# Kernel optimization log

Hardware: AMD Instinct MI355X
Metric: run time of the kernel (lower is better)

## Reference

```python
import jax, jax.numpy as jnp
import numpy as np

NEG_INF = -1e20

# Dims: s=512 samples, b=2048 background, t=32 trees, f=64 features, h=128 hidden, y=1
S, B, T, F, H, Y = 512, 2048, 32, 64, 128, 1


def setup_inputs() -> dict:
    key = jax.random.key(0)
    ks = jax.random.split(key, 8)
    X = jax.random.normal(ks[0], (S, F), dtype=jnp.float32)
    background_X = jax.random.normal(ks[1], (B, F), dtype=jnp.float32)
    background_y = jax.random.normal(ks[2], (B, Y), dtype=jnp.float32)
    neighbors_hot = jax.random.randint(ks[3], (S, B, T), 0, 2).astype(jnp.bool_)
    # encoder params: Linear(F->H), Tanh, Linear(H->H)  (n_layers=2)
    W1 = jax.random.normal(ks[4], (F, H), dtype=jnp.float32) / np.sqrt(F)
    b1 = jnp.zeros((H,), dtype=jnp.float32)
    W2 = jax.random.normal(ks[5], (H, H), dtype=jnp.float32) / np.sqrt(H)
    b2 = jnp.zeros((H,), dtype=jnp.float32)
    return {"X": X, "background_X": background_X, "background_y": background_y,
            "neighbors_hot": neighbors_hot, "W1": W1, "b1": b1, "W2": W2, "b2": b2}


def reference(X, background_X, background_y, neighbors_hot, W1, b1, W2, b2):
    def encode(x):
        return jnp.tanh(x @ W1 + b1) @ W2 + b2  # Linear-Tanh-Linear

    X_enc = encode(X)                    # (s, h)
    bg_enc = encode(background_X)        # (b, h)
    dots = X_enc @ bg_enc.T              # (s, b)
    # broadcast over trees + mask, softmax over background axis
    scores = jnp.where(neighbors_hot, dots[:, :, None], NEG_INF)  # (s, b, t)
    first_alphas = jax.nn.softmax(scores, axis=1)                 # (s, b, t)
    first_leaf_xs = jnp.einsum('sbt,bf->stf', first_alphas, background_X)
    first_leaf_y = jnp.einsum('sbt,by->sty', first_alphas, background_y)
    return first_leaf_xs, first_leaf_y, first_alphas
```

## Files before the change

### kernel.cpp

```cpp
#include <hip/hip_runtime.h>
#include <hip/hip_bf16.h>

#define NS 512
#define NB 2048
#define NT 32
#define NF 64
#define NH 128
#define NFX 80
#define PSTR 81

#define OY  ((size_t)NS * NT * NF)
#define OA  (OY + (size_t)NS * NT)

#define ENC_B  1280
#define TR_B   32

typedef __attribute__((ext_vector_type(8))) short bf16x8;
typedef __attribute__((ext_vector_type(4))) float f32x4;

__device__ __forceinline__ unsigned short f2bfu(float x) {
    __hip_bfloat16 h = __float2bfloat16(x);
    return __builtin_bit_cast(unsigned short, h);
}

__device__ __forceinline__ unsigned int pack16_bytes(uint4 v) {
    unsigned int r = 0;
    unsigned int xs[4] = {v.x, v.y, v.z, v.w};
    #pragma unroll
    for (int i = 0; i < 4; ++i) {
        unsigned int x = xs[i];
        unsigned int t = (x | ((x & 0x7F7F7F7Fu) + 0x7F7F7F7Fu)) & 0x80808080u;
        t >>= 7;
        unsigned int n = (t | (t >> 7) | (t >> 14) | (t >> 21)) & 0xFu;
        r |= n << (i * 4);
    }
    return r;
}

__global__ __launch_bounds__(256) void prep2_k(
        const float* __restrict__ X, const float* __restrict__ bgX,
        const float* __restrict__ bgy,
        const float* __restrict__ W1, const float* __restrict__ b1,
        const float* __restrict__ W2, const float* __restrict__ b2,
        float* __restrict__ enc, unsigned short* __restrict__ bgXT2) {
    __shared__ float cbuf[64 * 65];
    const int blk = blockIdx.x;
    const int tid = threadIdx.x;

    if (blk < ENC_B) {
        const int r0 = blk * 2;
        float* xr = cbuf;
        float* hr = cbuf + 128;
        if (tid < 128) {
            int r = tid >> 6, c = tid & 63;
            int row = r0 + r;
            const float* src = (row < NS) ? (X + (size_t)row * NF)
                                          : (bgX + (size_t)(row - NS) * NF);
            xr[r * 64 + c] = src[c];
        }
        __syncthreads();
        const int j = tid & 127, h = tid >> 7;
        const float* xh = xr + h * 64;
        float a1 = b1[j];
        #pragma unroll 4
        for (int f = 0; f < NF; ++f)
            a1 = fmaf(xh[f], W1[f * NH + j], a1);
        hr[h * 128 + j] = tanhf(a1);
        __syncthreads();
        const float* hh = hr + h * 128;
        float a2 = b2[j];
        #pragma unroll 4
        for (int k = 0; k < NH; ++k)
            a2 = fmaf(hh[k], W2[k * NH + j], a2);
        enc[(size_t)(r0 + h) * NH + j] = a2;
        return;
    }

    {
        const int bb0 = blk - ENC_B;
        const int b0 = bb0 * 64;
        float (*t_lds)[65] = (float(*)[65])cbuf;
        #pragma unroll
        for (int it = 0; it < 4; ++it) {
            int idx = (it * 256 + tid) * 4;
            int r = idx >> 6, c = idx & 63;
            *(float4*)(&t_lds[r][c]) = *(const float4*)(bgX + (size_t)(b0 + r) * NF + c);
        }
        __syncthreads();
        uint4* fb = (uint4*)bgXT2;
        const int c2 = tid >> 7;
        const int cg = bb0 * 2 + c2;
        for (int idx = tid & 127; idx < 320; idx += 128) {
            const int n = idx >> 6, l = idx & 63;
            const int lo = l & 15, hi = l >> 4;
            union { unsigned short u[8]; uint4 q; } pk;
            if (n < 4) {
                #pragma unroll
                for (int jj = 0; jj < 8; ++jj)
                    pk.u[jj] = f2bfu(t_lds[c2 * 32 + hi * 8 + jj][n * 16 + lo]);
            } else {
                #pragma unroll
                for (int jj = 0; jj < 8; ++jj) {
                    if (lo == 0)      pk.u[jj] = f2bfu(bgy[b0 + c2 * 32 + hi * 8 + jj]);
                    else if (lo == 1) pk.u[jj] = 0x3F80;
                    else              pk.u[jj] = 0;
                }
            }
            fb[((size_t)cg * 5 + n) * 64 + l] = pk.q;
        }
    }
}

__global__ __launch_bounds__(256) void dots_k(const float* __restrict__ Xe,
        const float* __restrict__ Be, float* __restrict__ dots) {
    __shared__ float At[64 * 68];
    __shared__ float Bt[64 * 68];
    const int s0 = blockIdx.y * 64, b0 = blockIdx.x * 64;
    const int tid = threadIdx.x;
    const int ts = tid >> 4, tb = tid & 15;
    float acc[4][4] = {};
    for (int kt = 0; kt < 2; ++kt) {
        __syncthreads();
        #pragma unroll
        for (int it = 0; it < 4; ++it) {
            int idx = tid * 4 + it * 1024;
            int r = idx >> 6, k = idx & 63;
            *(float4*)(&At[r * 68 + k]) = *(const float4*)(Xe + (size_t)(s0 + r) * NH + kt * 64 + k);
            float4 bvv = *(const float4*)(Be + (size_t)(b0 + r) * NH + kt * 64 + k);
            Bt[(k + 0) * 68 + r] = bvv.x;
            Bt[(k + 1) * 68 + r] = bvv.y;
            Bt[(k + 2) * 68 + r] = bvv.z;
            Bt[(k + 3) * 68 + r] = bvv.w;
        }
        __syncthreads();
        #pragma unroll 4
        for (int k = 0; k < 64; ++k) {
            float4 bq = *(const float4*)(&Bt[k * 68 + tb * 4]);
            float a[4];
            #pragma unroll
            for (int i = 0; i < 4; ++i) a[i] = At[(ts + 16 * i) * 68 + k];
            #pragma unroll
            for (int i = 0; i < 4; ++i) {
                acc[i][0] = fmaf(a[i], bq.x, acc[i][0]);
                acc[i][1] = fmaf(a[i], bq.y, acc[i][1]);
                acc[i][2] = fmaf(a[i], bq.z, acc[i][2]);
                acc[i][3] = fmaf(a[i], bq.w, acc[i][3]);
            }
        }
    }
    #pragma unroll
    for (int i = 0; i < 4; ++i) {
        float4 v = make_float4(acc[i][0], acc[i][1], acc[i][2], acc[i][3]);
        *(float4*)(&dots[(size_t)(s0 + ts + 16 * i) * NB + b0 + tb * 4]) = v;
    }
}

__global__ __launch_bounds__(256) void fusedA_k(const void* __restrict__ mask,
        float* __restrict__ dots, const unsigned short* __restrict__ bgXT2,
        unsigned int* __restrict__ pmask32,
        float* __restrict__ rden_g, float* __restrict__ out) {
    __shared__ __align__(16) unsigned int mrow[NB];
    __shared__ __align__(16) unsigned short e_bf[NB];
    __shared__ float part[3 * NT * PSTR];
    __shared__ float wmax[4];
    __shared__ float rden_l[NT];
    __shared__ float ytmp[NT];

    const int s = blockIdx.x;
    const int tid = threadIdx.x;
    const int lane = tid & 63, w = tid >> 6;
    const int lo = lane & 15, hi = lane >> 4;

    float* drow = dots + (size_t)s * NB;
    float4 d0 = *(const float4*)(drow + tid * 8);
    float4 d1 = *(const float4*)(drow + tid * 8 + 4);
    int isbyte;
    {
        uint4 v = ((const uint4*)mask)[w * 64 + lane];
        isbyte = (__ballot(((v.x | v.y | v.z | v.w) & 0xFFFFFF00u) != 0u) != 0ull);
    }
    if (isbyte) {
        const char* base = (const char*)mask + (size_t)s * 65536 + w * 16384;
        #pragma unroll 4
        for (int k = 0; k < 16; ++k) {
            uint4 q = *(const uint4*)(base + k * 1024 + lane * 16);
            unsigned int p = pack16_bytes(q);
            unsigned int p1 = (unsigned int)__shfl_down((int)p, 1, 64);
            if ((lane & 1) == 0)
                mrow[w * 512 + k * 32 + (lane >> 1)] = p | (p1 << 16);
        }
    } else {
        const char* base = (const char*)mask + (size_t)s * 262144 + w * 65536;
        for (int k = 0; k < 64; ++k) {
            uint4 v = *(const uint4*)(base + k * 1024 + lane * 16);
            unsigned int r = (v.x ? 1u : 0u) | (v.y ? 2u : 0u) |
                             (v.z ? 4u : 0u) | (v.w ? 8u : 0u);
            r |= ((unsigned int)__shfl_down((int)r, 1, 64)) << 4;
            r |= ((unsigned int)__shfl_down((int)r, 2, 64)) << 8;
            r |= ((unsigned int)__shfl_down((int)r, 4, 64)) << 16;
            if ((lane & 7) == 0)
                mrow[w * 512 + k * 8 + (lane >> 3)] = r;
        }
    }

    float pmax = fmaxf(fmaxf(fmaxf(d0.x, d0.y), fmaxf(d0.z, d0.w)),
                       fmaxf(fmaxf(d1.x, d1.y), fmaxf(d1.z, d1.w)));
    #pragma unroll
    for (int off = 32; off >= 1; off >>= 1)
        pmax = fmaxf(pmax, __shfl_xor(pmax, off, 64));
    if (lane == 0) wmax[w] = pmax;
    __syncthreads();
    const float Ms = fmaxf(fmaxf(wmax[0], wmax[1]), fmaxf(wmax[2], wmax[3]));
    float ev[8] = {d0.x, d0.y, d0.z, d0.w, d1.x, d1.y, d1.z, d1.w};
    union { unsigned short u[8]; uint4 q; } epk;
    #pragma unroll
    for (int q = 0; q < 8; ++q) { ev[q] = __expf(ev[q] - Ms); epk.u[q] = f2bfu(ev[q]); }
    *(float4*)(drow + tid * 8)     = make_float4(ev[0], ev[1], ev[2], ev[3]);
    *(float4*)(drow + tid * 8 + 4) = make_float4(ev[4], ev[5], ev[6], ev[7]);
    *(uint4*)(&e_bf[tid * 8]) = epk.q;
    unsigned int* pmg = pmask32 + (size_t)s * NB;
    *(uint4*)(pmg + tid * 4)          = *(const uint4*)(&mrow[tid * 4]);
    *(uint4*)(pmg + (tid + 256) * 4)  = *(const uint4*)(&mrow[(tid + 256) * 4]);
    __syncthreads();

    f32x4 acc[2][5] = {};
    const uint4* fb = (const uint4*)bgXT2;
    #pragma unroll 2
    for (int ks = 0; ks < 16; ++ks) {
        const int bb = w * 512 + ks * 32 + hi * 8;
        uint4 ew4 = *(const uint4*)(&e_bf[bb]);
        uint4 m0 = *(const uint4*)(&mrow[bb]);
        uint4 m1 = *(const uint4*)(&mrow[bb + 4]);
        unsigned int ew[4] = {ew4.x, ew4.y, ew4.z, ew4.w};
        unsigned int mv[8] = {m0.x, m0.y, m0.z, m0.w, m1.x, m1.y, m1.z, m1.w};
        unsigned int A0[4], A1[4];
        #pragma unroll
        for (int p = 0; p < 4; ++p) {
            unsigned int mlo = mv[2 * p]     >> lo;
            unsigned int mhi = mv[2 * p + 1] >> lo;
            unsigned int k0 = ((mlo & 1u)       ? 0x0000FFFFu : 0u) |
                              ((mhi & 1u)       ? 0xFFFF0000u : 0u);
            unsigned int k1 = ((mlo & 0x10000u) ? 0x0000FFFFu : 0u) |
                              ((mhi & 0x10000u) ? 0xFFFF0000u : 0u);
            A0[p] = ew[p] & k0;
            A1[p] = ew[p] & k1;
        }
        bf16x8 a0 = __builtin_bit_cast(bf16x8, make_uint4(A0[0], A0[1], A0[2], A0[3]));
        bf16x8 a1 = __builtin_bit_cast(bf16x8, make_uint4(A1[0], A1[1], A1[2], A1[3]));
        const uint4* fr = fb + ((size_t)(w * 16 + ks) * 5) * 64 + lane;
        #pragma unroll
        for (int n = 0; n < 5; ++n) {
            uint4 bv = fr[n * 64];
            bf16x8 bfr = __builtin_bit_cast(bf16x8, bv);
            acc[0][n] = __builtin_amdgcn_mfma_f32_16x16x32_bf16(a0, bfr, acc[0][n], 0, 0, 0);
            acc[1][n] = __builtin_amdgcn_mfma_f32_16x16x32_bf16(a1, bfr, acc[1][n], 0, 0, 0);
        }
    }

    if (w > 0) {
        #pragma unroll
        for (int m = 0; m < 2; ++m)
            #pragma unroll
            for (int n = 0; n < 5; ++n)
                #pragma unroll
                for (int r = 0; r < 4; ++r) {
                    int t = m * 16 + hi * 4 + r, f = n * 16 + lo;
                    part[(w - 1) * (NT * PSTR) + t * PSTR + f] = acc[m][n][r];
                }
    }
    __syncthreads();
    if (w == 0) {
        #pragma unroll
        for (int m = 0; m < 2; ++m)
            #pragma unroll
            for (int r = 0; r < 4; ++r) {
                int t = m * 16 + hi * 4 + r;
                int o = t * PSTR + 64 + lo;
                float tot = acc[m][4][r] + part[o] + part[NT * PSTR + o] + part[2 * NT * PSTR + o];
                if (lo == 0) ytmp[t] = tot;
                if (lo == 1) rden_l[t] = (tot > 0.f) ? 1.f / tot : 0.f;
            }
    }
    __syncthreads();
    if (w == 0) {
        float* xout = out + (size_t)s * NT * NF;
        #pragma unroll
        for (int m = 0; m < 2; ++m)
            #pragma unroll
            for (int n = 0; n < 4; ++n)
                #pragma unroll
                for (int r = 0; r < 4; ++r) {
                    int t = m * 16 + hi * 4 + r, f = n * 16 + lo;
                    int o = t * PSTR + f;
                    float tot = acc[m][n][r] + part[o] + part[NT * PSTR + o] + part[2 * NT * PSTR + o];
                    xout[t * NF + f] = tot * rden_l[t];
                }
    }
    if (tid < 32) {
        out[OY + (size_t)s * NT + tid] = ytmp[tid] * rden_l[tid];
        rden_g[(size_t)s * NT + tid] = rden_l[tid];
    }
}

__global__ __launch_bounds__(256) void alphas_k(const float* __restrict__ e,
        const unsigned int* __restrict__ pmask32, const float* __restrict__ rden_g,
        float* __restrict__ out) {
    const int tid = threadIdx.x;
    const int blk = blockIdx.x;
    const int s = blk >> 3;
    const int tq = tid & 7;
    const f32x4 rd4 = *(const f32x4*)(rden_g + (size_t)s * NT + tq * 4);
    const float* erow = e + (size_t)s * NB;
    const unsigned int* mr = pmask32 + (size_t)s * NB;
    float* aout = out + OA + (size_t)s * NB * NT;
    const int b0 = (blk & 7) * 256 + (tid >> 3);

    float ev[8];
    unsigned int mv[8];
    #pragma unroll
    for (int j = 0; j < 8; ++j) {
        ev[j] = erow[b0 + j * 32];
        mv[j] = mr[b0 + j * 32] >> (tq * 4);
    }
    #pragma unroll
    for (int j = 0; j < 8; ++j) {
        const int b = b0 + j * 32;
        f32x4 v;
        v.x = (mv[j] & 1u) ? ev[j] * rd4.x : 0.f;
        v.y = (mv[j] & 2u) ? ev[j] * rd4.y : 0.f;
        v.z = (mv[j] & 4u) ? ev[j] * rd4.z : 0.f;
        v.w = (mv[j] & 8u) ? ev[j] * rd4.w : 0.f;
        *(f32x4*)(aout + (size_t)b * NT + tq * 4) = v;
    }
}

extern "C" void kernel_launch(void* const* d_in, const int* in_sizes, int n_in,
                              void* d_out, int out_size, void* d_ws, size_t ws_size,
                              hipStream_t stream) {
    (void)in_sizes; (void)n_in; (void)out_size; (void)ws_size;
    const float* X   = (const float*)d_in[0];
    const float* bgX = (const float*)d_in[1];
    const float* bgy = (const float*)d_in[2];
    const void*  nh  = d_in[3];
    const float* W1  = (const float*)d_in[4];
    const float* b1v = (const float*)d_in[5];
    const float* W2  = (const float*)d_in[6];
    const float* b2v = (const float*)d_in[7];
    float* out = (float*)d_out;
    char* ws = (char*)d_ws;

    float* enc = (float*)(ws + 4096);
    float* rden_g = (float*)(ws + 4096);
    float* Xe = enc;
    float* Be = enc + (size_t)NS * NH;
    float* dots = (float*)(ws + 4096 + (size_t)(NS + NB) * NH * 4);
    unsigned int* pmask32 = (unsigned int*)((char*)dots + (size_t)NS * NB * 4);
    unsigned short* bgXT2 = (unsigned short*)((char*)pmask32 + (size_t)NS * NB * 4);

    prep2_k<<<ENC_B + TR_B, 256, 0, stream>>>(X, bgX, bgy, W1, b1v, W2, b2v, enc, bgXT2);
    dots_k<<<dim3(NB / 64, NS / 64), 256, 0, stream>>>(Xe, Be, dots);
    fusedA_k<<<NS, 256, 0, stream>>>(nh, dots, bgXT2, pmask32, rden_g, out);
    alphas_k<<<NS * 8, 256, 0, stream>>>(dots, pmask32, rden_g, out);
}
```

Baseline: 115.2 us.

## Drop packed-mask buffer; reread raw mask in alphas kernel and shrink reduction LDS

fusedA_k no longer writes a packed per-sample bitmask to global memory. alphas_k now rereads the original byte or int mask directly, which removes the pmask32 round trip and a barrier. The cross-wave partial reduction uses one LDS buffer reused over three sequential rounds instead of three buffers, cutting LDS use to raise occupancy at the cost of extra barriers. The mask loads in fusedA_k are batched eight at a time to get more loads in flight. In exchange alphas_k reads the full byte mask (32 MB) rather than the 4 MB packed copy.

New measurement: 123.9 us. +7.5%, slower.

```diff
diff --git a/kernel.cpp b/kernel.cpp
--- a/kernel.cpp
+++ b/kernel.cpp
@@ -35,6 +35,11 @@
         r |= n << (i * 4);
     }
     return r;
+}
+
+__device__ __forceinline__ int detect_isbyte(const void* mask, int tid) {
+    uint4 v = ((const uint4*)mask)[tid & 255];
+    return (__ballot(((v.x | v.y | v.z | v.w) & 0xFFFFFF00u) != 0u) != 0ull);
 }
 
 __global__ __launch_bounds__(256) void prep2_k(
@@ -157,11 +162,10 @@
 
 __global__ __launch_bounds__(256) void fusedA_k(const void* __restrict__ mask,
         float* __restrict__ dots, const unsigned short* __restrict__ bgXT2,
-        unsigned int* __restrict__ pmask32,
         float* __restrict__ rden_g, float* __restrict__ out) {
     __shared__ __align__(16) unsigned int mrow[NB];
     __shared__ __align__(16) unsigned short e_bf[NB];
-    __shared__ float part[3 * NT * PSTR];
+    __shared__ float part[NT * PSTR];
     __shared__ float wmax[4];
     __shared__ float rden_l[NT];
     __shared__ float ytmp[NT];
@@ -174,20 +178,22 @@
     float* drow = dots + (size_t)s * NB;
     float4 d0 = *(const float4*)(drow + tid * 8);
     float4 d1 = *(const float4*)(drow + tid * 8 + 4);
-    int isbyte;
-    {
-        uint4 v = ((const uint4*)mask)[w * 64 + lane];
-        isbyte = (__ballot(((v.x | v.y | v.z | v.w) & 0xFFFFFF00u) != 0u) != 0ull);
-    }
+    const int isbyte = detect_isbyte(mask, tid);
     if (isbyte) {
         const char* base = (const char*)mask + (size_t)s * 65536 + w * 16384;
-        #pragma unroll 4
-        for (int k = 0; k < 16; ++k) {
-            uint4 q = *(const uint4*)(base + k * 1024 + lane * 16);
-            unsigned int p = pack16_bytes(q);
-            unsigned int p1 = (unsigned int)__shfl_down((int)p, 1, 64);
-            if ((lane & 1) == 0)
-                mrow[w * 512 + k * 32 + (lane >> 1)] = p | (p1 << 16);
+        #pragma unroll
+        for (int g = 0; g < 2; ++g) {
+            uint4 q[8];
+            #pragma unroll
+            for (int k = 0; k < 8; ++k)
+                q[k] = *(const uint4*)(base + (g * 8 + k) * 1024 + lane * 16);
+            #pragma unroll
+            for (int k = 0; k < 8; ++k) {
+                unsigned int p = pack16_bytes(q[k]);
+                unsigned int p1 = (unsigned int)__shfl_down((int)p, 1, 64);
+                if ((lane & 1) == 0)
+                    mrow[w * 512 + (g * 8 + k) * 32 + (lane >> 1)] = p | (p1 << 16);
+            }
         }
     } else {
         const char* base = (const char*)mask + (size_t)s * 262144 + w * 65536;
@@ -218,10 +224,6 @@
     *(float4*)(drow + tid * 8)     = make_float4(ev[0], ev[1], ev[2], ev[3]);
     *(float4*)(drow + tid * 8 + 4) = make_float4(ev[4], ev[5], ev[6], ev[7]);
     *(uint4*)(&e_bf[tid * 8]) = epk.q;
-    unsigned int* pmg = pmask32 + (size_t)s * NB;
-    *(uint4*)(pmg + tid * 4)          = *(const uint4*)(&mrow[tid * 4]);
-    *(uint4*)(pmg + (tid + 256) * 4)  = *(const uint4*)(&mrow[(tid + 256) * 4]);
-    __syncthreads();
 
     f32x4 acc[2][5] = {};
     const uint4* fb = (const uint4*)bgXT2;
@@ -257,28 +259,40 @@
         }
     }
 
-    if (w > 0) {
-        #pragma unroll
-        for (int m = 0; m < 2; ++m)
-            #pragma unroll
-            for (int n = 0; n < 5; ++n)
-                #pragma unroll
-                for (int r = 0; r < 4; ++r) {
-                    int t = m * 16 + hi * 4 + r, f = n * 16 + lo;
-                    part[(w - 1) * (NT * PSTR) + t * PSTR + f] = acc[m][n][r];
-                }
-    }
-    __syncthreads();
+    for (int src = 1; src < 4; ++src) {
+        __syncthreads();
+        if (w == src) {
+            #pragma unroll
+            for (int m = 0; m < 2; ++m)
+                #pragma unroll
+                for (int n = 0; n < 5; ++n)
+                    #pragma unroll
+                    for (int r = 0; r < 4; ++r) {
+                        int t = m * 16 + hi * 4 + r, f = n * 16 + lo;
+                        part[t * PSTR + f] = acc[m][n][r];
+                    }
+        }
+        __syncthreads();
+        if (w == 0) {
+            #pragma unroll
+            for (int m = 0; m < 2; ++m)
+                #pragma unroll
+                for (int n = 0; n < 5; ++n)
+                    #pragma unroll
+                    for (int r = 0; r < 4; ++r) {
+                        int t = m * 16 + hi * 4 + r, f = n * 16 + lo;
+                        acc[m][n][r] += part[t * PSTR + f];
+                    }
+        }
+    }
     if (w == 0) {
         #pragma unroll
         for (int m = 0; m < 2; ++m)
             #pragma unroll
             for (int r = 0; r < 4; ++r) {
                 int t = m * 16 + hi * 4 + r;
-                int o = t * PSTR + 64 + lo;
-                float tot = acc[m][4][r] + part[o] + part[NT * PSTR + o] + part[2 * NT * PSTR + o];
-                if (lo == 0) ytmp[t] = tot;
-                if (lo == 1) rden_l[t] = (tot > 0.f) ? 1.f / tot : 0.f;
+                if (lo == 0) ytmp[t] = acc[m][4][r];
+                if (lo == 1) rden_l[t] = (acc[m][4][r] > 0.f) ? 1.f / acc[m][4][r] : 0.f;
             }
     }
     __syncthreads();
@@ -291,9 +305,7 @@
                 #pragma unroll
                 for (int r = 0; r < 4; ++r) {
                     int t = m * 16 + hi * 4 + r, f = n * 16 + lo;
-                    int o = t * PSTR + f;
-                    float tot = acc[m][n][r] + part[o] + part[NT * PSTR + o] + part[2 * NT * PSTR + o];
-                    xout[t * NF + f] = tot * rden_l[t];
+                    xout[t * NF + f] = acc[m][n][r] * rden_l[t];
                 }
     }
     if (tid < 32) {
@@ -302,8 +314,8 @@
     }
 }
 
-__global__ __launch_bounds__(256) void alphas_k(const float* __restrict__ e,
-        const unsigned int* __restrict__ pmask32, const float* __restrict__ rden_g,
+__global__ __launch_bounds__(256) void alphas_k(const void* __restrict__ mask,
+        const float* __restrict__ e, const float* __restrict__ rden_g,
         float* __restrict__ out) {
     const int tid = threadIdx.x;
     const int blk = blockIdx.x;
@@ -311,26 +323,48 @@
     const int tq = tid & 7;
     const f32x4 rd4 = *(const f32x4*)(rden_g + (size_t)s * NT + tq * 4);
     const float* erow = e + (size_t)s * NB;
-    const unsigned int* mr = pmask32 + (size_t)s * NB;
     float* aout = out + OA + (size_t)s * NB * NT;
     const int b0 = (blk & 7) * 256 + (tid >> 3);
+    const int isbyte = detect_isbyte(mask, tid);
 
     float ev[8];
-    unsigned int mv[8];
-    #pragma unroll
-    for (int j = 0; j < 8; ++j) {
-        ev[j] = erow[b0 + j * 32];
-        mv[j] = mr[b0 + j * 32] >> (tq * 4);
-    }
-    #pragma unroll
-    for (int j = 0; j < 8; ++j) {
-        const int b = b0 + j * 32;
-        f32x4 v;
-        v.x = (mv[j] & 1u) ? ev[j] * rd4.x : 0.f;
-        v.y = (mv[j] & 2u) ? ev[j] * rd4.y : 0.f;
-        v.z = (mv[j] & 4u) ? ev[j] * rd4.z : 0.f;
-        v.w = (mv[j] & 8u) ? ev[j] * rd4.w : 0.f;
-        *(f32x4*)(aout + (size_t)b * NT + tq * 4) = v;
+    #pragma unroll
+    for (int j = 0; j < 8; ++j) ev[j] = erow[b0 + j * 32];
+
+    if (isbyte) {
+        const unsigned char* base = (const unsigned char*)mask
+                                  + (size_t)s * 65536 + (size_t)(blk & 7) * 8192;
+        uchar4 m4[8];
+        #pragma unroll
+        for (int j = 0; j < 8; ++j)
+            m4[j] = *(const uchar4*)(base + j * 1024 + tid * 4);
+        #pragma unroll
+        for (int j = 0; j < 8; ++j) {
+            const int b = b0 + j * 32;
+            f32x4 v;
+            v.x = m4[j].x ? ev[j] * rd4.x : 0.f;
+            v.y = m4[j].y ? ev[j] * rd4.y : 0.f;
+            v.z = m4[j].z ? ev[j] * rd4.z : 0.f;
+            v.w = m4[j].w ? ev[j] * rd4.w : 0.f;
+            *(f32x4*)(aout + (size_t)b * NT + tq * 4) = v;
+        }
+    } else {
+        const uint4* mi = (const uint4*)mask;
+        const size_t mbase = (size_t)s * 16384 + (size_t)(blk & 7) * 2048;
+        uint4 m4[8];
+        #pragma unroll
+        for (int j = 0; j < 8; ++j)
+            m4[j] = mi[mbase + j * 256 + tid];
+        #pragma unroll
+        for (int j = 0; j < 8; ++j) {
+            const int b = b0 + j * 32;
+            f32x4 v;
+            v.x = m4[j].x ? ev[j] * rd4.x : 0.f;
+            v.y = m4[j].y ? ev[j] * rd4.y : 0.f;
+            v.z = m4[j].z ? ev[j] * rd4.z : 0.f;
+            v.w = m4[j].w ? ev[j] * rd4.w : 0.f;
+            *(f32x4*)(aout + (size_t)b * NT + tq * 4) = v;
+        }
     }
 }
 
@@ -354,11 +388,10 @@
     float* Xe = enc;
     float* Be = enc + (size_t)NS * NH;
     float* dots = (float*)(ws + 4096 + (size_t)(NS + NB) * NH * 4);
-    unsigned int* pmask32 = (unsigned int*)((char*)dots + (size_t)NS * NB * 4);
-    unsigned short* bgXT2 = (unsigned short*)((char*)pmask32 + (size_t)NS * NB * 4);
+    unsigned short* bgXT2 = (unsigned short*)((char*)dots + (size_t)NS * NB * 4);
 
     prep2_k<<<ENC_B + TR_B, 256, 0, stream>>>(X, bgX, bgy, W1, b1v, W2, b2v, enc, bgXT2);
     dots_k<<<dim3(NB / 64, NS / 64), 256, 0, stream>>>(Xe, Be, dots);
-    fusedA_k<<<NS, 256, 0, stream>>>(nh, dots, bgXT2, pmask32, rden_g, out);
-    alphas_k<<<NS * 8, 256, 0, stream>>>(dots, pmask32, rden_g, out);
-}
+    fusedA_k<<<NS, 256, 0, stream>>>(nh, dots, bgXT2, rden_g, out);
+    alphas_k<<<NS * 8, 256, 0, stream>>>(nh, dots, rden_g, out);
+}
```
